# Kernel tuning notes

Hardware: AMD Instinct MI355X
Metric: run time of the kernel (lower is better)

## Reference

```python
import jax, jax.numpy as jnp
import numpy as np
from jax import lax

K = 3          # kernel size
STRIDE = 1
PAD = 1
DIL = 1

def setup_inputs() -> dict:
    key = jax.random.key(0)
    k1, k2 = jax.random.split(key)
    N, C, H, W = 8, 256, 56, 56
    Cw = 32                      # weight channels = C // share_planes (share=8)
    L = H * W                    # stride 1, pad 1 -> same spatial size
    inp = jax.random.normal(k1, (N, C, H, W), dtype=jnp.float32)
    weight = jax.random.normal(k2, (N, Cw, K * K, L), dtype=jnp.float32)
    return {"input": inp, "weight": weight}

def reference(input, weight):
    N, C, H, W = input.shape
    _, Cw, KK, L = weight.shape
    share = C // Cw
    # Extract KxK patches (zero padding). Output: [N, C*K*K, Ho, Wo],
    # feature dim ordered channel-outermost, matching torch unfold.
    patches = lax.conv_general_dilated_patches(
        input, filter_shape=(K, K), window_strides=(STRIDE, STRIDE),
        padding=[(PAD, PAD), (PAD, PAD)], rhs_dilation=(DIL, DIL))
    Ho, Wo = patches.shape[2], patches.shape[3]
    # [N, Cw, share, K*K, L]
    patches = patches.reshape(N, Cw, share, KK, Ho * Wo)
    # broadcast weight over share channels, reduce over kernel taps
    out = jnp.einsum('ngskl,ngkl->ngsl', patches, weight)
    return out.reshape(N, C, Ho, Wo)
```

## Files before the change

### kernel.cpp

```cpp
#include <hip/hip_runtime.h>


#define HH 56
#define WW 56
#define LL 3136
#define CW 32
#define SHARE 8
#define CC 256
#define NN 8

__global__ __launch_bounds__(256) void agg_kernel(const float* __restrict__ in,
                                                  const float* __restrict__ wt,
                                                  float* __restrict__ out) {
    const int l = blockIdx.x * 256 + threadIdx.x;
    const int g = blockIdx.y;
    const int n = blockIdx.z;
    if (l >= LL) return;
    const int h = l / WW;
    const int w = l - h * WW;

    const float* wp = wt + (((size_t)n * CW + g) * 9) * LL + l;
    float w9[9];
#pragma unroll
    for (int kk = 0; kk < 9; ++kk) w9[kk] = wp[(size_t)kk * LL];

    int off[9];
    bool val[9];
#pragma unroll
    for (int kk = 0; kk < 9; ++kk) {
        const int hh = h + kk / 3 - 1;
        const int ww = w + kk % 3 - 1;
        val[kk] = ((unsigned)hh < (unsigned)HH) && ((unsigned)ww < (unsigned)WW);
        off[kk] = hh * WW + ww;
    }

    const int c0 = g * SHARE;
    const float* ip = in + ((size_t)n * CC + c0) * LL;
    float* op = out + ((size_t)n * CC + c0) * LL;
#pragma unroll
    for (int s = 0; s < SHARE; ++s) {
        float acc = 0.f;
#pragma unroll
        for (int kk = 0; kk < 9; ++kk) {
            const float v = val[kk] ? ip[(size_t)s * LL + off[kk]] : 0.f;
            acc = fmaf(v, w9[kk], acc);
        }
        op[(size_t)s * LL + l] = acc;
    }
}

extern "C" void kernel_launch(void* const* d_in, const int* in_sizes, int n_in,
                              void* d_out, int out_size, void* d_ws, size_t ws_size,
                              hipStream_t stream) {
    const float* in = (const float*)d_in[0];
    const float* wt = (const float*)d_in[1];
    float* out = (float*)d_out;
    dim3 grid((LL + 255) / 256, CW, NN);
    agg_kernel<<<grid, 256, 0, stream>>>(in, wt, out);
}
```

Before: 21.72 us.

## Stage 14-row input bands in LDS and compute four pixels per thread

Each block now handles one 14-row band of a (batch, group) pair. It loads the 8 shared input channels, plus a one-row halo, into LDS with float4 loads, and zeroes the halo columns. Each thread then reads its weights as float4 and computes four adjacent output pixels for all 8 channels from LDS, writing float4 outputs. The aim is to replace the 9 predicated scattered global loads per output with coalesced vector loads and LDS reuse. In exchange it adds a barrier, about 40 KB of LDS per block, and leaves 60 of 256 threads idle in the compute phase.

Result: slower. 24.84 us (+14.4%).

```diff
diff --git a/kernel.cpp b/kernel.cpp
--- a/kernel.cpp
+++ b/kernel.cpp
@@ -5,47 +5,89 @@
 #define WW 56
 #define LL 3136
 #define CW 32
-#define SHARE 8
 #define CC 256
 #define NN 8
+#define RBAND 14
+#define SROWS 16
+#define LDSTR 68
+#define CHSTR (SROWS * LDSTR)
+#define COLOFF 4
 
 __global__ __launch_bounds__(256) void agg_kernel(const float* __restrict__ in,
                                                   const float* __restrict__ wt,
                                                   float* __restrict__ out) {
-    const int l = blockIdx.x * 256 + threadIdx.x;
-    const int g = blockIdx.y;
-    const int n = blockIdx.z;
-    if (l >= LL) return;
-    const int h = l / WW;
-    const int w = l - h * WW;
+    __shared__ float lds[8 * CHSTR];
 
-    const float* wp = wt + (((size_t)n * CW + g) * 9) * LL + l;
-    float w9[9];
+    const unsigned b    = blockIdx.x;
+    const unsigned band = b & 3u;
+    const unsigned ng   = b >> 2;
+    const unsigned g    = ng & 31u;
+    const unsigned n    = ng >> 5;
+    const unsigned t    = threadIdx.x;
+    const unsigned h0   = band * RBAND;
+
+    const unsigned qc = (t < 196u) ? t : 195u;
+    const unsigned hb = qc / 14u;
+    const unsigned wq = (qc - hb * 14u) * 4u;
+    const unsigned h  = h0 + hb;
+    const unsigned lq = h * WW + wq;
+
+    const float* wp = wt + (((size_t)n * CW + g) * 9u) * LL + lq;
+    float4 wv[9];
 #pragma unroll
-    for (int kk = 0; kk < 9; ++kk) w9[kk] = wp[(size_t)kk * LL];
+    for (int kk = 0; kk < 9; ++kk) wv[kk] = *(const float4*)(wp + (size_t)kk * LL);
 
-    int off[9];
-    bool val[9];
+    const unsigned grp  = t >> 5;
+    const unsigned lane = t & 31u;
+    const unsigned c    = g * 8u + grp;
+    const float*   ip   = in + ((size_t)n * CC + c) * LL;
 #pragma unroll
-    for (int kk = 0; kk < 9; ++kk) {
-        const int hh = h + kk / 3 - 1;
-        const int ww = w + kk % 3 - 1;
-        val[kk] = ((unsigned)hh < (unsigned)HH) && ((unsigned)ww < (unsigned)WW);
-        off[kk] = hh * WW + ww;
+    for (int j = 0; j < 7; ++j) {
+        const unsigned k    = lane + j * 32u;
+        const unsigned grow = k / 14u;
+        const unsigned gcol = (k - grow * 14u) * 4u;
+        const int      gr   = (int)(h0 + grow) - 1;
+        float4 v = make_float4(0.f, 0.f, 0.f, 0.f);
+        if ((unsigned)gr < HH) v = *(const float4*)(ip + (size_t)gr * WW + gcol);
+        *(float4*)&lds[grp * CHSTR + grow * LDSTR + COLOFF + gcol] = v;
     }
+    {
+        const unsigned ch   = t >> 5;
+        const unsigned rr   = (t >> 1) & 15u;
+        const unsigned ccol = (t & 1u) ? 60u : 3u;
+        lds[ch * CHSTR + rr * LDSTR + ccol] = 0.f;
+    }
+    __syncthreads();
 
-    const int c0 = g * SHARE;
-    const float* ip = in + ((size_t)n * CC + c0) * LL;
-    float* op = out + ((size_t)n * CC + c0) * LL;
+    if (t < 196u) {
+        float* op = out + ((size_t)n * CC + g * 8u) * LL + lq;
 #pragma unroll
-    for (int s = 0; s < SHARE; ++s) {
-        float acc = 0.f;
+        for (int ch = 0; ch < 8; ++ch) {
+            float4 a = make_float4(0.f, 0.f, 0.f, 0.f);
 #pragma unroll
-        for (int kk = 0; kk < 9; ++kk) {
-            const float v = val[kk] ? ip[(size_t)s * LL + off[kk]] : 0.f;
-            acc = fmaf(v, w9[kk], acc);
+            for (int dr = 0; dr < 3; ++dr) {
+                const float* lp = &lds[ch * CHSTR + (hb + dr) * LDSTR + COLOFF + wq];
+                const float  r0 = lp[-1];
+                const float4 c4 = *(const float4*)lp;
+                const float  r5 = lp[4];
+                const float4 wa = wv[3 * dr + 0];
+                const float4 wb = wv[3 * dr + 1];
+                const float4 wc = wv[3 * dr + 2];
+                a.x = fmaf(r0,   wa.x, a.x);
+                a.y = fmaf(c4.x, wa.y, a.y);
+                a.z = fmaf(c4.y, wa.z, a.z);
+                a.w = fmaf(c4.z, wa.w, a.w);
+                a.x = fmaf(c4.x, wb.x, a.x);
+                a.y = fmaf(c4.y, wb.y, a.y);
+                a.z = fmaf(c4.z, wb.z, a.z);
+                a.w = fmaf(c4.w, wb.w, a.w);
+                a.x = fmaf(c4.y, wc.x, a.x);
+                a.y = fmaf(c4.z, wc.y, a.y);
+                a.z = fmaf(c4.w, wc.z, a.z);
+                a.w = fmaf(r5,   wc.w, a.w);
+            }
+            *(float4*)(op + (size_t)ch * LL) = a;
         }
-        op[(size_t)s * LL + l] = acc;
     }
 }
 
@@ -55,6 +97,5 @@
     const float* in = (const float*)d_in[0];
     const float* wt = (const float*)d_in[1];
     float* out = (float*)d_out;
-    dim3 grid((LL + 255) / 256, CW, NN);
-    agg_kernel<<<grid, 256, 0, stream>>>(in, wt, out);
+    agg_kernel<<<dim3(NN * CW * 4), dim3(256), 0, stream>>>(in, wt, out);
 }
```

## Map one wavefront per image row and share horizontal taps via lane shuffles

Applied to the files above, without the earlier changes.

Remaps the grid so each 64-lane wavefront covers one 56-wide image row, with 4 rows per block. Each thread loads only the three vertical neighbours per channel and gets the left and right taps through cross-lane shuffles. This cuts global load instructions from 9 to 3 per channel per output and drops the per-tap bounds arithmetic. In exchange, 8 of every 64 lanes are idle (clamped and masked on store), and the shuffles add cross-lane traffic.

Measured after the change: 20.77 us. -4.4%, faster.

```diff
diff --git a/kernel.cpp b/kernel.cpp
--- a/kernel.cpp
+++ b/kernel.cpp
@@ -5,47 +5,72 @@
 #define WW 56
 #define LL 3136
 #define CW 32
-#define SHARE 8
 #define CC 256
 #define NN 8
 
 __global__ __launch_bounds__(256) void agg_kernel(const float* __restrict__ in,
                                                   const float* __restrict__ wt,
                                                   float* __restrict__ out) {
-    const int l = blockIdx.x * 256 + threadIdx.x;
-    const int g = blockIdx.y;
-    const int n = blockIdx.z;
-    if (l >= LL) return;
-    const int h = l / WW;
-    const int w = l - h * WW;
+    const unsigned t    = threadIdx.x;
+    const unsigned wid  = t >> 6;
+    const unsigned lane = t & 63u;
+    const unsigned b    = blockIdx.x;
+    const unsigned hb   = b % 14u;
+    const unsigned ng   = b / 14u;
+    const unsigned g    = ng & 31u;
+    const unsigned n    = ng >> 5;
+    const unsigned h    = hb * 4u + wid;
+    const unsigned w    = lane;
+    const unsigned wcl  = (w < 55u) ? w : 55u;
+    const unsigned l    = h * WW + wcl;
 
-    const float* wp = wt + (((size_t)n * CW + g) * 9) * LL + l;
+    const float* wp = wt + (((size_t)n * CW + g) * 9u) * LL + l;
     float w9[9];
 #pragma unroll
-    for (int kk = 0; kk < 9; ++kk) w9[kk] = wp[(size_t)kk * LL];
+    for (int k = 0; k < 9; ++k) w9[k] = wp[(size_t)k * LL];
 
-    int off[9];
-    bool val[9];
+    const bool up = (h > 0), dn = (h < HH - 1);
+    const bool wz = (w == 0), we = (w >= 55u);
+    const float* ip = in  + ((size_t)n * CC + g * 8u) * LL + l;
+    float*       op = out + ((size_t)n * CC + g * 8u) * LL + l;
+
+    float cm[8], cc[8], cp[8];
 #pragma unroll
-    for (int kk = 0; kk < 9; ++kk) {
-        const int hh = h + kk / 3 - 1;
-        const int ww = w + kk % 3 - 1;
-        val[kk] = ((unsigned)hh < (unsigned)HH) && ((unsigned)ww < (unsigned)WW);
-        off[kk] = hh * WW + ww;
+    for (int ch = 0; ch < 8; ++ch) {
+        const float* p = ip + (size_t)ch * LL;
+        cm[ch] = up ? p[-(int)WW] : 0.f;
+        cc[ch] = p[0];
+        cp[ch] = dn ? p[WW] : 0.f;
     }
 
-    const int c0 = g * SHARE;
-    const float* ip = in + ((size_t)n * CC + c0) * LL;
-    float* op = out + ((size_t)n * CC + c0) * LL;
 #pragma unroll
-    for (int s = 0; s < SHARE; ++s) {
+    for (int ch = 0; ch < 8; ++ch) {
         float acc = 0.f;
-#pragma unroll
-        for (int kk = 0; kk < 9; ++kk) {
-            const float v = val[kk] ? ip[(size_t)s * LL + off[kk]] : 0.f;
-            acc = fmaf(v, w9[kk], acc);
+        {
+            float lf = __shfl_up(cm[ch], 1);
+            float rt = __shfl_down(cm[ch], 1);
+            lf = wz ? 0.f : lf;  rt = we ? 0.f : rt;
+            acc = fmaf(lf, w9[0], acc);
+            acc = fmaf(cm[ch], w9[1], acc);
+            acc = fmaf(rt, w9[2], acc);
         }
-        op[(size_t)s * LL + l] = acc;
+        {
+            float lf = __shfl_up(cc[ch], 1);
+            float rt = __shfl_down(cc[ch], 1);
+            lf = wz ? 0.f : lf;  rt = we ? 0.f : rt;
+            acc = fmaf(lf, w9[3], acc);
+            acc = fmaf(cc[ch], w9[4], acc);
+            acc = fmaf(rt, w9[5], acc);
+        }
+        {
+            float lf = __shfl_up(cp[ch], 1);
+            float rt = __shfl_down(cp[ch], 1);
+            lf = wz ? 0.f : lf;  rt = we ? 0.f : rt;
+            acc = fmaf(lf, w9[6], acc);
+            acc = fmaf(cp[ch], w9[7], acc);
+            acc = fmaf(rt, w9[8], acc);
+        }
+        if (w < 56u) op[(size_t)ch * LL] = acc;
     }
 }
 
@@ -55,6 +80,5 @@
     const float* in = (const float*)d_in[0];
     const float* wt = (const float*)d_in[1];
     float* out = (float*)d_out;
-    dim3 grid((LL + 255) / 256, CW, NN);
-    agg_kernel<<<grid, 256, 0, stream>>>(in, wt, out);
+    agg_kernel<<<dim3(NN * CW * 14), dim3(256), 0, stream>>>(in, wt, out);
 }
```

## Tile 4x56 row bands per wavefront with float4 loads and shuffle-based halo exchange

Applied to the files above, without the earlier changes.

Each block now handles one (n, group) pair and a 4-row band, with one wavefront per share channel. Each lane computes 4 adjacent outputs using float4 loads, and neighbouring rows and columns are fetched through cross-lane shuffles instead of nine scattered scalar loads with bounds checks. The aim is to cut redundant global and cache traffic and per-element address arithmetic. In exchange the weights are now loaded once per wavefront, i.e. 8 times per block, the last 8 lanes of every wave do no useful work, and the code depends on exact 56-wide geometry.

Result: faster. 20.21 us (-6.9%).

```diff
diff --git a/kernel.cpp b/kernel.cpp
--- a/kernel.cpp
+++ b/kernel.cpp
@@ -5,47 +5,84 @@
 #define WW 56
 #define LL 3136
 #define CW 32
-#define SHARE 8
 #define CC 256
 #define NN 8
 
-__global__ __launch_bounds__(256) void agg_kernel(const float* __restrict__ in,
+__device__ __forceinline__ float4 shfl_up4(float4 v, int d) {
+    return make_float4(__shfl_up(v.x, d), __shfl_up(v.y, d),
+                       __shfl_up(v.z, d), __shfl_up(v.w, d));
+}
+__device__ __forceinline__ float4 shfl_down4(float4 v, int d) {
+    return make_float4(__shfl_down(v.x, d), __shfl_down(v.y, d),
+                       __shfl_down(v.z, d), __shfl_down(v.w, d));
+}
+
+__global__ __launch_bounds__(512) void agg_kernel(const float* __restrict__ in,
                                                   const float* __restrict__ wt,
                                                   float* __restrict__ out) {
-    const int l = blockIdx.x * 256 + threadIdx.x;
-    const int g = blockIdx.y;
-    const int n = blockIdx.z;
-    if (l >= LL) return;
-    const int h = l / WW;
-    const int w = l - h * WW;
+    const unsigned t    = threadIdx.x;
+    const unsigned wid  = t >> 6;
+    const unsigned lane = t & 63u;
+    const unsigned b    = blockIdx.x;
+    const unsigned band = b % 14u;
+    const unsigned ng   = b / 14u;
+    const unsigned g    = ng & 31u;
+    const unsigned n    = ng >> 5;
 
-    const float* wp = wt + (((size_t)n * CW + g) * 9) * LL + l;
-    float w9[9];
+    const unsigned rq = (lane < 56u) ? lane : 55u;
+    const unsigned r  = rq / 14u;
+    const unsigned q  = rq - r * 14u;
+    const unsigned h  = band * 4u + r;
+    const unsigned w4 = q * 4u;
+    const unsigned l  = h * WW + w4;
+
+    const float* wp = wt + (((size_t)n * CW + g) * 9u) * LL + l;
+    float4 wv[9];
 #pragma unroll
-    for (int kk = 0; kk < 9; ++kk) w9[kk] = wp[(size_t)kk * LL];
+    for (int k = 0; k < 9; ++k) wv[k] = *(const float4*)(wp + (size_t)k * LL);
 
-    int off[9];
-    bool val[9];
-#pragma unroll
-    for (int kk = 0; kk < 9; ++kk) {
-        const int hh = h + kk / 3 - 1;
-        const int ww = w + kk % 3 - 1;
-        val[kk] = ((unsigned)hh < (unsigned)HH) && ((unsigned)ww < (unsigned)WW);
-        off[kk] = hh * WW + ww;
-    }
+    const unsigned c = g * 8u + wid;
+    const float* ip = in + ((size_t)n * CC + c) * LL;
+    const float4 c4 = *(const float4*)(ip + l);
+    float4 hm = make_float4(0.f, 0.f, 0.f, 0.f);
+    float4 hp = make_float4(0.f, 0.f, 0.f, 0.f);
+    if (r == 0u && h > 0u)       hm = *(const float4*)(ip + l - WW);
+    if (r == 3u && h < HH - 1u)  hp = *(const float4*)(ip + l + WW);
 
-    const int c0 = g * SHARE;
-    const float* ip = in + ((size_t)n * CC + c0) * LL;
-    float* op = out + ((size_t)n * CC + c0) * LL;
-#pragma unroll
-    for (int s = 0; s < SHARE; ++s) {
-        float acc = 0.f;
-#pragma unroll
-        for (int kk = 0; kk < 9; ++kk) {
-            const float v = val[kk] ? ip[(size_t)s * LL + off[kk]] : 0.f;
-            acc = fmaf(v, w9[kk], acc);
-        }
-        op[(size_t)s * LL + l] = acc;
+    const float4 sm = shfl_up4(c4, 14);
+    const float4 sp = shfl_down4(c4, 14);
+    const float4 rm = (r == 0u) ? hm : sm;
+    const float4 rp = (r == 3u) ? hp : sp;
+
+    const bool qz = (q == 0u), qe = (q == 13u);
+    float lm = __shfl_up(rm.w, 1), lc = __shfl_up(c4.w, 1), lp = __shfl_up(rp.w, 1);
+    float em = __shfl_down(rm.x, 1), ec = __shfl_down(c4.x, 1), ep = __shfl_down(rp.x, 1);
+    if (qz) { lm = 0.f; lc = 0.f; lp = 0.f; }
+    if (qe) { em = 0.f; ec = 0.f; ep = 0.f; }
+
+    float4 a = make_float4(0.f, 0.f, 0.f, 0.f);
+    a.x = fmaf(lm,   wv[0].x, a.x); a.y = fmaf(rm.x, wv[0].y, a.y);
+    a.z = fmaf(rm.y, wv[0].z, a.z); a.w = fmaf(rm.z, wv[0].w, a.w);
+    a.x = fmaf(rm.x, wv[1].x, a.x); a.y = fmaf(rm.y, wv[1].y, a.y);
+    a.z = fmaf(rm.z, wv[1].z, a.z); a.w = fmaf(rm.w, wv[1].w, a.w);
+    a.x = fmaf(rm.y, wv[2].x, a.x); a.y = fmaf(rm.z, wv[2].y, a.y);
+    a.z = fmaf(rm.w, wv[2].z, a.z); a.w = fmaf(em,   wv[2].w, a.w);
+    a.x = fmaf(lc,   wv[3].x, a.x); a.y = fmaf(c4.x, wv[3].y, a.y);
+    a.z = fmaf(c4.y, wv[3].z, a.z); a.w = fmaf(c4.z, wv[3].w, a.w);
+    a.x = fmaf(c4.x, wv[4].x, a.x); a.y = fmaf(c4.y, wv[4].y, a.y);
+    a.z = fmaf(c4.z, wv[4].z, a.z); a.w = fmaf(c4.w, wv[4].w, a.w);
+    a.x = fmaf(c4.y, wv[5].x, a.x); a.y = fmaf(c4.z, wv[5].y, a.y);
+    a.z = fmaf(c4.w, wv[5].z, a.z); a.w = fmaf(ec,   wv[5].w, a.w);
+    a.x = fmaf(lp,   wv[6].x, a.x); a.y = fmaf(rp.x, wv[6].y, a.y);
+    a.z = fmaf(rp.y, wv[6].z, a.z); a.w = fmaf(rp.z, wv[6].w, a.w);
+    a.x = fmaf(rp.x, wv[7].x, a.x); a.y = fmaf(rp.y, wv[7].y, a.y);
+    a.z = fmaf(rp.z, wv[7].z, a.z); a.w = fmaf(rp.w, wv[7].w, a.w);
+    a.x = fmaf(rp.y, wv[8].x, a.x); a.y = fmaf(rp.z, wv[8].y, a.y);
+    a.z = fmaf(rp.w, wv[8].z, a.z); a.w = fmaf(ep,   wv[8].w, a.w);
+
+    if (lane < 56u) {
+        float* op = out + ((size_t)n * CC + c) * LL + l;
+        *(float4*)op = a;
     }
 }
 
@@ -55,6 +92,5 @@
     const float* in = (const float*)d_in[0];
     const float* wt = (const float*)d_in[1];
     float* out = (float*)d_out;
-    dim3 grid((LL + 255) / 256, CW, NN);
-    agg_kernel<<<grid, 256, 0, stream>>>(in, wt, out);
+    agg_kernel<<<dim3(NN * CW * 14), dim3(512), 0, stream>>>(in, wt, out);
 }
```
